# Kernel tuning notes

Measured on AMD Instinct MI355X. Metric: run time of the kernel, lower is better.

## Reference

```python
import jax, jax.numpy as jnp
import numpy as np

N = 100_000   # nodes
E = 1_200_000 # edges
D = 64        # in_dim
H = 64        # hidden_dim
B = 1000      # graphs in batch
C = 10        # num_classes
TOPO = 64     # topo_dim
BN_EPS = 1e-5


def setup_inputs() -> dict:
    key = jax.random.key(0)
    ks = jax.random.split(key, 24)
    x = jax.random.normal(ks[0], (N, D), dtype=jnp.float32)
    edge_index = jax.random.randint(ks[1], (2, E), 0, N, dtype=jnp.int32)
    # sorted graph ids; force last id = B-1 so batch.max()+1 == B (matches torch path)
    batch = jnp.sort(jax.random.randint(ks[2], (N,), 0, B, dtype=jnp.int32)).at[-1].set(B - 1)
    topo = jax.random.normal(ks[3], (B, TOPO), dtype=jnp.float32)
    s = 0.05
    return {
        "x": x, "edge_index": edge_index, "batch": batch, "topo": topo,
        # conv1 MLP: Linear(D,H) -> BN(H) -> ReLU -> Linear(H,H) -> ReLU
        "W1a": jax.random.normal(ks[4], (D, H)) * s, "b1a": jax.random.normal(ks[5], (H,)) * s,
        "g1": 1.0 + jax.random.normal(ks[6], (H,)) * s, "be1": jax.random.normal(ks[7], (H,)) * s,
        "m1": jax.random.normal(ks[8], (H,)) * s, "v1": 0.5 + jax.random.uniform(ks[9], (H,)),
        "W1b": jax.random.normal(ks[10], (H, H)) * s, "b1b": jax.random.normal(ks[11], (H,)) * s,
        # conv2 MLP: Linear(H,H) -> BN(H) -> ReLU
        "W2": jax.random.normal(ks[12], (H, H)) * s, "b2": jax.random.normal(ks[13], (H,)) * s,
        "g2": 1.0 + jax.random.normal(ks[14], (H,)) * s, "be2": jax.random.normal(ks[15], (H,)) * s,
        "m2": jax.random.normal(ks[16], (H,)) * s, "v2": 0.5 + jax.random.uniform(ks[17], (H,)),
        # topo_net: Linear(TOPO,H) -> ReLU
        "Wt": jax.random.normal(ks[18], (TOPO, H)) * s, "bt": jax.random.normal(ks[19], (H,)) * s,
        # classifier: Linear(2H, C)
        "Wc": jax.random.normal(ks[20], (2 * H, C)) * s, "bc": jax.random.normal(ks[21], (C,)) * s,
    }


def _bn_eval(v, g, b, m, var):
    # BatchNorm1d in eval mode: affine with running stats
    return g * (v - m) * jax.lax.rsqrt(var + BN_EPS) + b


def _gin_agg(h, src, dst):
    # GINConv (eps=0): (1+eps)*x_i + sum_{j->i} x_j ; scatter-add over dst
    return h + jax.ops.segment_sum(h[src], dst, num_segments=N)


def reference(x, edge_index, batch, topo,
              W1a, b1a, g1, be1, m1, v1, W1b, b1b,
              W2, b2, g2, be2, m2, v2, Wt, bt, Wc, bc):
    src, dst = edge_index[0], edge_index[1]
    # conv1: MLP(agg(x)) = Lin -> BN -> ReLU -> Lin -> ReLU; outer relu from forward
    h = _gin_agg(x, src, dst)                              # [N, D]
    h = jax.nn.relu(_bn_eval(h @ W1a + b1a, g1, be1, m1, v1))
    h = jax.nn.relu(h @ W1b + b1b)                         # [N, H]
    h = jax.nn.relu(h)                                     # F.relu(conv1(...))
    # dropout(p=0.5) is identity in eval mode
    # conv2: Lin -> BN -> ReLU, then outer relu
    h = _gin_agg(h, src, dst)                              # [N, H]
    h = jax.nn.relu(_bn_eval(h @ W2 + b2, g2, be2, m2, v2))
    h = jax.nn.relu(h)
    # global_add_pool: sum nodes per graph
    x_struct = jax.ops.segment_sum(h, batch, num_segments=B)   # [B, H]
    # topo already [B, TOPO] => all reshape/pad branches are no-ops
    x_topo = jax.nn.relu(topo @ Wt + bt)                   # [B, H]
    combined = jnp.concatenate([x_struct, x_topo], axis=1) # [B, 2H]
    return combined @ Wc + bc                              # [B, C]
```

## Files before the change

kernel.cpp:

```cpp
#include <hip/hip_runtime.h>

#define N_NODES 100000
#define N_EDGES 1200000
#define DIM     64
#define BGRAPHS 1000
#define NCLASS  10
#define BN_EPS  1e-5f

#define NBUCK   256
#define NPB     391
#define MAGIC   10984572u
#define CHUNK   8192
#define NBLK_P  147
#define SCAN_N  (NBUCK * NBLK_P)
#define CAP     8192

typedef __attribute__((ext_vector_type(8))) short   bfx8;
typedef __attribute__((ext_vector_type(4))) float   f32x4;
typedef __attribute__((ext_vector_type(8))) unsigned short u16x8;

__device__ __forceinline__ unsigned short f2bf(float f) {
    unsigned u = __builtin_bit_cast(unsigned, f);
    unsigned r = (u + 0x7FFFu + ((u >> 16) & 1u)) >> 16;
    return (unsigned short)r;
}
__device__ __forceinline__ float bf2f(unsigned short h) {
    unsigned u = ((unsigned)h) << 16;
    return __builtin_bit_cast(float, u);
}

__global__ void convert_kernel(const float* __restrict__ x, unsigned short* __restrict__ xb,
                               float* __restrict__ xs) {
    int i = blockIdx.x * blockDim.x + threadIdx.x;
    const int n8 = N_NODES * DIM / 8;
    if (i < n8) {
        float4 a = ((const float4*)x)[i * 2];
        float4 b = ((const float4*)x)[i * 2 + 1];
        u16x8 o;
        o[0] = f2bf(a.x); o[1] = f2bf(a.y); o[2] = f2bf(a.z); o[3] = f2bf(a.w);
        o[4] = f2bf(b.x); o[5] = f2bf(b.y); o[6] = f2bf(b.z); o[7] = f2bf(b.w);
        ((u16x8*)xb)[i] = o;
    }
    if (i < BGRAPHS * DIM) xs[i] = 0.f;
}

__global__ __launch_bounds__(256) void histA_kernel(const int* __restrict__ ei,
                                                    int* __restrict__ hist) {
    __shared__ int cnt[NBUCK];
    int t = threadIdx.x, blk = blockIdx.x;
    cnt[t] = 0;
    __syncthreads();
    int e0 = blk * CHUNK;
    for (int i = t; i < CHUNK; i += 256) {
        int e = e0 + i;
        if (e >= N_EDGES) break;
        unsigned d = (unsigned)ei[N_EDGES + e];
        int b = __umulhi(d, MAGIC);
        atomicAdd(&cnt[b], 1);
    }
    __syncthreads();
    hist[t * NBLK_P + blk] = cnt[t];
}

__global__ __launch_bounds__(256) void scan1_kernel(const int* __restrict__ in,
                                                    int* __restrict__ outp,
                                                    int* __restrict__ bsum, int n) {
    __shared__ int tmp[256];
    int t = threadIdx.x;
    int base = blockIdx.x * 1024;
    int v[4]; int s = 0;
    #pragma unroll
    for (int j = 0; j < 4; ++j) {
        int idx = base + t * 4 + j;
        v[j] = (idx < n) ? in[idx] : 0;
        s += v[j];
    }
    tmp[t] = s;
    __syncthreads();
    for (int off = 1; off < 256; off <<= 1) {
        int a = (t >= off) ? tmp[t - off] : 0;
        __syncthreads();
        tmp[t] += a;
        __syncthreads();
    }
    int excl = tmp[t] - s;
    if (t == 255) bsum[blockIdx.x] = tmp[255];
    int run = excl;
    #pragma unroll
    for (int j = 0; j < 4; ++j) {
        int idx = base + t * 4 + j;
        if (idx < n) outp[idx] = run;
        run += v[j];
    }
}

__global__ __launch_bounds__(128) void scan2_kernel(int* __restrict__ bsum, int nb) {
    __shared__ int tmp[128];
    int t = threadIdx.x;
    int v = (t < nb) ? bsum[t] : 0;
    tmp[t] = v;
    __syncthreads();
    for (int off = 1; off < 128; off <<= 1) {
        int a = (t >= off) ? tmp[t - off] : 0;
        __syncthreads();
        tmp[t] += a;
        __syncthreads();
    }
    if (t < nb) bsum[t] = tmp[t] - v;
}

__global__ void scan3_kernel(int* __restrict__ arr, const int* __restrict__ bsum, int n) {
    int i = blockIdx.x * blockDim.x + threadIdx.x;
    if (i < n) arr[i] += bsum[i >> 10];
}

__global__ __launch_bounds__(256) void part_kernel(const int* __restrict__ ei,
                                                   const int* __restrict__ base,
                                                   int* __restrict__ srcbuf,
                                                   unsigned short* __restrict__ dstlbuf) {
    __shared__ int cur[NBUCK];
    int t = threadIdx.x, blk = blockIdx.x;
    cur[t] = base[t * NBLK_P + blk];
    __syncthreads();
    int e0 = blk * CHUNK;
    for (int i = t; i < CHUNK; i += 256) {
        int e = e0 + i;
        if (e >= N_EDGES) break;
        unsigned d = (unsigned)ei[N_EDGES + e];
        int s = ei[e];
        int b = __umulhi(d, MAGIC);
        int pos = atomicAdd(&cur[b], 1);
        srcbuf[pos] = s;
        dstlbuf[pos] = (unsigned short)(d - b * NPB);
    }
}

__global__ __launch_bounds__(256) void refine_kernel(const int* __restrict__ srcbuf,
                                                     const unsigned short* __restrict__ dstlbuf,
                                                     const int* __restrict__ base,
                                                     int* __restrict__ csr_src,
                                                     int* __restrict__ rowptr) {
    __shared__ int cnt[NPB + 1];
    __shared__ int cur[NPB + 1];
    __shared__ int tmp[256];
    __shared__ int outb[CAP];
    int t = threadIdx.x, b = blockIdx.x;
    int beg = base[b * NBLK_P];
    int end = (b == NBUCK - 1) ? N_EDGES : base[(b + 1) * NBLK_P];

    for (int i = t; i < NPB + 1; i += 256) cnt[i] = 0;
    __syncthreads();
    for (int i = beg + t; i < end; i += 256)
        atomicAdd(&cnt[dstlbuf[i]], 1);
    __syncthreads();

    int i0 = 2 * t, i1 = 2 * t + 1;
    int v0 = (i0 < NPB) ? cnt[i0] : 0;
    int v1 = (i1 < NPB) ? cnt[i1] : 0;
    int s = v0 + v1;
    tmp[t] = s;
    __syncthreads();
    for (int off = 1; off < 256; off <<= 1) {
        int a = (t >= off) ? tmp[t - off] : 0;
        __syncthreads();
        tmp[t] += a;
        __syncthreads();
    }
    int excl = tmp[t] - s;
    if (i0 < NPB) cur[i0] = excl;
    if (i1 < NPB) cur[i1] = excl + v0;
    {
        int g0 = b * NPB + i0;
        if (i0 < NPB && g0 < N_NODES) rowptr[g0] = beg + excl;
        int g1 = b * NPB + i1;
        if (i1 < NPB && g1 < N_NODES) rowptr[g1] = beg + excl + v0;
    }
    if (b == NBUCK - 1 && t == 0) rowptr[N_NODES] = N_EDGES;
    __syncthreads();

    for (int i = beg + t; i < end; i += 256) {
        int dl = dstlbuf[i];
        int pos = atomicAdd(&cur[dl], 1);
        if (pos < CAP) outb[pos] = srcbuf[i];
    }
    __syncthreads();

    int nb = end - beg; if (nb > CAP) nb = CAP;
    for (int i = t; i < nb; i += 256) csr_src[beg + i] = outb[i];
}

__global__ __launch_bounds__(256) void gather_kernel(const unsigned short* __restrict__ feat,
                                                     const int* __restrict__ rowptr,
                                                     const int* __restrict__ csr_src,
                                                     unsigned short* __restrict__ out) {
    int t = threadIdx.x;
    int node = blockIdx.x * 32 + (t >> 3);
    int q = t & 7;
    if (node >= N_NODES) return;
    const u16x8* f8 = (const u16x8*)feat;
    u16x8 sv = f8[(long long)node * 8 + q];
    float acc[8];
    #pragma unroll
    for (int j = 0; j < 8; ++j) acc[j] = bf2f(sv[j]);
    int beg = rowptr[node], end = rowptr[node + 1];
    int k = beg;
    int sn = (k < end) ? csr_src[k] : 0;
    while (k < end) {
        int sc = sn;
        ++k;
        if (k < end) sn = csr_src[k];
        u16x8 v = f8[(long long)sc * 8 + q];
        #pragma unroll
        for (int j = 0; j < 8; ++j) acc[j] += bf2f(v[j]);
    }
    u16x8 o;
    #pragma unroll
    for (int j = 0; j < 8; ++j) o[j] = f2bf(acc[j]);
    ((u16x8*)out)[(long long)node * 8 + q] = o;
}

__device__ __forceinline__ bfx8 load_wfrag(const float* __restrict__ W, int kt, int q, int col) {
    bfx8 f;
    #pragma unroll
    for (int j = 0; j < 8; ++j)
        f[j] = (short)f2bf(W[(kt * 32 + q * 8 + j) * 64 + col]);
    return f;
}

__global__ __launch_bounds__(256) void mlp1_kernel(
    const unsigned short* __restrict__ h0,
    const float* __restrict__ W1a, const float* __restrict__ b1a,
    const float* __restrict__ g1,  const float* __restrict__ be1,
    const float* __restrict__ m1,  const float* __restrict__ v1,
    const float* __restrict__ W1b, const float* __restrict__ b1b,
    unsigned short* __restrict__ h2) {
    __shared__ unsigned short h1t[4][16 * 72];
    __shared__ unsigned short outt[4][16 * 64];

    int t = threadIdx.x;
    int w = t >> 6, lane = t & 63;
    int m = lane & 15, q = lane >> 4;
    int row0 = blockIdx.x * 64 + w * 16;

    bfx8 wa[4][2], wb[4][2];
    #pragma unroll
    for (int nt = 0; nt < 4; ++nt) {
        #pragma unroll
        for (int kt = 0; kt < 2; ++kt) {
            wa[nt][kt] = load_wfrag(W1a, kt, q, nt * 16 + m);
            wb[nt][kt] = load_wfrag(W1b, kt, q, nt * 16 + m);
        }
    }
    float A1[4], B1[4], B2c[4];
    #pragma unroll
    for (int nt = 0; nt < 4; ++nt) {
        int c = nt * 16 + m;
        float s = g1[c] * rsqrtf(v1[c] + BN_EPS);
        A1[nt] = s;
        B1[nt] = b1a[c] * s + (be1[c] - m1[c] * s);
        B2c[nt] = b1b[c];
    }

    int rowA = row0 + m;
    if (rowA > N_NODES - 1) rowA = N_NODES - 1;
    const bfx8* ap = (const bfx8*)(h0 + (long long)rowA * 64);
    bfx8 a0 = ap[q];
    bfx8 a1 = ap[4 + q];
    f32x4 acc[4];
    #pragma unroll
    for (int nt = 0; nt < 4; ++nt) {
        acc[nt] = (f32x4){0.f, 0.f, 0.f, 0.f};
        acc[nt] = __builtin_amdgcn_mfma_f32_16x16x32_bf16(a0, wa[nt][0], acc[nt], 0, 0, 0);
        acc[nt] = __builtin_amdgcn_mfma_f32_16x16x32_bf16(a1, wa[nt][1], acc[nt], 0, 0, 0);
    }
    #pragma unroll
    for (int nt = 0; nt < 4; ++nt)
        #pragma unroll
        for (int r = 0; r < 4; ++r) {
            float v = fmaxf(acc[nt][r] * A1[nt] + B1[nt], 0.f);
            h1t[w][(q * 4 + r) * 72 + nt * 16 + m] = f2bf(v);
        }
    __syncthreads();

    const bfx8* hp = (const bfx8*)&h1t[w][m * 72];
    bfx8 c0 = hp[q];
    bfx8 c1 = hp[4 + q];
    f32x4 acc2[4];
    #pragma unroll
    for (int nt = 0; nt < 4; ++nt) {
        acc2[nt] = (f32x4){0.f, 0.f, 0.f, 0.f};
        acc2[nt] = __builtin_amdgcn_mfma_f32_16x16x32_bf16(c0, wb[nt][0], acc2[nt], 0, 0, 0);
        acc2[nt] = __builtin_amdgcn_mfma_f32_16x16x32_bf16(c1, wb[nt][1], acc2[nt], 0, 0, 0);
    }
    #pragma unroll
    for (int nt = 0; nt < 4; ++nt)
        #pragma unroll
        for (int r = 0; r < 4; ++r) {
            float v = fmaxf(acc2[nt][r] + B2c[nt], 0.f);
            outt[w][(q * 4 + r) * 64 + nt * 16 + m] = f2bf(v);
        }
    __syncthreads();

    #pragma unroll
    for (int i = lane; i < 128; i += 64) {
        int rr = i >> 3, cc = i & 7;
        int rg = row0 + rr;
        if (rg < N_NODES)
            ((float4*)h2)[(long long)rg * 8 + cc] = *(const float4*)&outt[w][rr * 64 + cc * 8];
    }
}

__global__ __launch_bounds__(256) void mlp2_kernel(
    const unsigned short* __restrict__ h3,
    const float* __restrict__ W2, const float* __restrict__ b2,
    const float* __restrict__ g2, const float* __restrict__ be2,
    const float* __restrict__ m2, const float* __restrict__ v2,
    const int* __restrict__ batch,
    float* __restrict__ xs) {
    __shared__ float pool[64 * 64];
    __shared__ int bts[64];

    int t = threadIdx.x;
    int w = t >> 6, lane = t & 63;
    int m = lane & 15, q = lane >> 4;
    int row0b = blockIdx.x * 64;
    int row0 = row0b + w * 16;

    bfx8 wf[4][2];
    #pragma unroll
    for (int nt = 0; nt < 4; ++nt)
        #pragma unroll
        for (int kt = 0; kt < 2; ++kt)
            wf[nt][kt] = load_wfrag(W2, kt, q, nt * 16 + m);
    float A[4], Bc[4];
    #pragma unroll
    for (int nt = 0; nt < 4; ++nt) {
        int c = nt * 16 + m;
        float s = g2[c] * rsqrtf(v2[c] + BN_EPS);
        A[nt] = s;
        Bc[nt] = b2[c] * s + (be2[c] - m2[c] * s);
    }
    if (t < 64) {
        int rg = row0b + t;
        bts[t] = (rg < N_NODES) ? batch[rg] : -1;
    }

    int rowA = row0 + m;
    if (rowA > N_NODES - 1) rowA = N_NODES - 1;
    const bfx8* ap = (const bfx8*)(h3 + (long long)rowA * 64);
    bfx8 a0 = ap[q];
    bfx8 a1 = ap[4 + q];
    f32x4 acc[4];
    #pragma unroll
    for (int nt = 0; nt < 4; ++nt) {
        acc[nt] = (f32x4){0.f, 0.f, 0.f, 0.f};
        acc[nt] = __builtin_amdgcn_mfma_f32_16x16x32_bf16(a0, wf[nt][0], acc[nt], 0, 0, 0);
        acc[nt] = __builtin_amdgcn_mfma_f32_16x16x32_bf16(a1, wf[nt][1], acc[nt], 0, 0, 0);
    }
    #pragma unroll
    for (int nt = 0; nt < 4; ++nt)
        #pragma unroll
        for (int r = 0; r < 4; ++r) {
            float v = fmaxf(acc[nt][r] * A[nt] + Bc[nt], 0.f);
            pool[(w * 16 + q * 4 + r) * 64 + nt * 16 + m] = v;
        }
    __syncthreads();

    int col = t & 63;
    int r0 = (t >> 6) * 16;
    int cb = bts[r0];
    float cur = 0.f;
    #pragma unroll
    for (int r = 0; r < 16; ++r) {
        int b = bts[r0 + r];
        if (b != cb) {
            if (cb >= 0) unsafeAtomicAdd(&xs[cb * 64 + col], cur);
            cb = b;
            cur = 0.f;
        }
        cur += pool[(r0 + r) * 64 + col];
    }
    if (cb >= 0) unsafeAtomicAdd(&xs[cb * 64 + col], cur);
}

__global__ __launch_bounds__(64) void head_kernel(
    const float* __restrict__ xs, const float* __restrict__ topo,
    const float* __restrict__ Wt, const float* __restrict__ bt,
    const float* __restrict__ Wc, const float* __restrict__ bc,
    float* __restrict__ out) {
    __shared__ float trow[64];
    __shared__ float comb[128];
    int b = blockIdx.x;
    int h = threadIdx.x;
    trow[h] = topo[b * 64 + h];
    __syncthreads();
    float acc = bt[h];
    #pragma unroll
    for (int k = 0; k < 64; ++k) acc += trow[k] * Wt[k * 64 + h];
    comb[h] = xs[b * 64 + h];
    comb[64 + h] = fmaxf(acc, 0.f);
    __syncthreads();
    if (h < NCLASS) {
        float o = bc[h];
        #pragma unroll
        for (int k = 0; k < 128; ++k) o += comb[k] * Wc[k * NCLASS + h];
        out[b * NCLASS + h] = o;
    }
}

extern "C" void kernel_launch(void* const* d_in, const int* in_sizes, int n_in,
                              void* d_out, int out_size, void* d_ws, size_t ws_size,
                              hipStream_t stream) {
    const float* x     = (const float*)d_in[0];
    const int*   ei    = (const int*)d_in[1];
    const int*   batch = (const int*)d_in[2];
    const float* topo  = (const float*)d_in[3];
    const float* W1a   = (const float*)d_in[4];
    const float* b1a   = (const float*)d_in[5];
    const float* g1    = (const float*)d_in[6];
    const float* be1   = (const float*)d_in[7];
    const float* m1    = (const float*)d_in[8];
    const float* v1    = (const float*)d_in[9];
    const float* W1b   = (const float*)d_in[10];
    const float* b1b   = (const float*)d_in[11];
    const float* W2    = (const float*)d_in[12];
    const float* b2    = (const float*)d_in[13];
    const float* g2    = (const float*)d_in[14];
    const float* be2   = (const float*)d_in[15];
    const float* m2    = (const float*)d_in[16];
    const float* v2    = (const float*)d_in[17];
    const float* Wt    = (const float*)d_in[18];
    const float* bt    = (const float*)d_in[19];
    const float* Wc    = (const float*)d_in[20];
    const float* bc    = (const float*)d_in[21];
    float* out = (float*)d_out;

    char* p = (char*)d_ws;
    unsigned short* xbf  = (unsigned short*)p; p += (size_t)N_NODES * DIM * 2;
    unsigned short* bufA = (unsigned short*)p; p += (size_t)N_NODES * DIM * 2;
    unsigned short* bufB = (unsigned short*)p; p += (size_t)N_NODES * DIM * 2;
    float* xs      = (float*)p; p += (size_t)BGRAPHS * DIM * 4;
    int*   rowptr  = (int*)p;   p += (size_t)(N_NODES + 16) * 4;
    int*   histc   = (int*)p;   p += (size_t)SCAN_N * 4;
    int*   base    = (int*)p;   p += (size_t)SCAN_N * 4;
    int*   bsum    = (int*)p;   p += 256 * 4;
    int*   srcbuf  = (int*)p;   p += (size_t)N_EDGES * 4;
    unsigned short* dstlbuf = (unsigned short*)p; p += (size_t)N_EDGES * 2;
    int*   csr_src = (int*)p;

    const int NB_C  = (N_NODES * DIM / 8 + 255) / 256;
    const int NB_S1 = (SCAN_N + 1023) / 1024;
    const int NB_S3 = (SCAN_N + 255) / 256;

    convert_kernel<<<NB_C, 256, 0, stream>>>(x, xbf, xs);
    histA_kernel<<<NBLK_P, 256, 0, stream>>>(ei, histc);
    scan1_kernel<<<NB_S1, 256, 0, stream>>>(histc, base, bsum, SCAN_N);
    scan2_kernel<<<1, 128, 0, stream>>>(bsum, NB_S1);
    scan3_kernel<<<NB_S3, 256, 0, stream>>>(base, bsum, SCAN_N);
    part_kernel<<<NBLK_P, 256, 0, stream>>>(ei, base, srcbuf, dstlbuf);
    refine_kernel<<<NBUCK, 256, 0, stream>>>(srcbuf, dstlbuf, base, csr_src, rowptr);

    gather_kernel<<<(N_NODES + 31) / 32, 256, 0, stream>>>(xbf, rowptr, csr_src, bufA);
    mlp1_kernel<<<(N_NODES + 63) / 64, 256, 0, stream>>>(
        bufA, W1a, b1a, g1, be1, m1, v1, W1b, b1b, bufB);
    gather_kernel<<<(N_NODES + 31) / 32, 256, 0, stream>>>(bufB, rowptr, csr_src, bufA);
    mlp2_kernel<<<(N_NODES + 63) / 64, 256, 0, stream>>>(
        bufA, W2, b2, g2, be2, m2, v2, batch, xs);
    head_kernel<<<BGRAPHS, 64, 0, stream>>>(xs, topo, Wt, bt, Wc, bc, out);
}
```

Baseline: 246.8 us.

## Fuse neighbor gather into MLP kernels and collapse CSR scan pipeline

Removes the standalone gather kernels and performs the CSR neighbor aggregation directly inside mlp1/mlp2, so the aggregated bf16 rows no longer round-trip through global memory. Each MFMA row lane now gathers 16 features across two 8-wide chunks, unrolled by two edges. Separately, the bf16 convert and edge histogram are merged into one launch, and the three-kernel scan is replaced by a single bucket-level scan plus atomic cursors in part_kernel. This cuts launches and intermediate traffic. In exchange, edge order within buckets becomes nondeterministic and gather parallelism per node drops (4 lanes instead of 8), which may expose more latency.

```diff
diff --git a/kernel.cpp b/kernel.cpp
--- a/kernel.cpp
+++ b/kernel.cpp
@@ -12,8 +12,8 @@
 #define MAGIC   10984572u
 #define CHUNK   8192
 #define NBLK_P  147
-#define SCAN_N  (NBUCK * NBLK_P)
 #define CAP     8192
+#define NB_C    3125
 
 typedef __attribute__((ext_vector_type(8))) short   bfx8;
 typedef __attribute__((ext_vector_type(4))) float   f32x4;
@@ -29,24 +29,67 @@
     return __builtin_bit_cast(float, u);
 }
 
-__global__ void convert_kernel(const float* __restrict__ x, unsigned short* __restrict__ xb,
-                               float* __restrict__ xs) {
-    int i = blockIdx.x * blockDim.x + threadIdx.x;
-    const int n8 = N_NODES * DIM / 8;
-    if (i < n8) {
-        float4 a = ((const float4*)x)[i * 2];
-        float4 b = ((const float4*)x)[i * 2 + 1];
-        u16x8 o;
-        o[0] = f2bf(a.x); o[1] = f2bf(a.y); o[2] = f2bf(a.z); o[3] = f2bf(a.w);
-        o[4] = f2bf(b.x); o[5] = f2bf(b.y); o[6] = f2bf(b.z); o[7] = f2bf(b.w);
-        ((u16x8*)xb)[i] = o;
-    }
-    if (i < BGRAPHS * DIM) xs[i] = 0.f;
-}
-
-__global__ __launch_bounds__(256) void histA_kernel(const int* __restrict__ ei,
-                                                    int* __restrict__ hist) {
+__global__ __launch_bounds__(256) void convhist_kernel(
+    const float* __restrict__ x, unsigned short* __restrict__ xb,
+    float* __restrict__ xs, const int* __restrict__ ei,
+    int* __restrict__ gpart) {
     __shared__ int cnt[NBUCK];
+    int t = threadIdx.x;
+    if (blockIdx.x < NBLK_P) {
+        int blk = blockIdx.x;
+        cnt[t] = 0;
+        __syncthreads();
+        int e0 = blk * CHUNK;
+        for (int i = t; i < CHUNK; i += 256) {
+            int e = e0 + i;
+            if (e >= N_EDGES) break;
+            unsigned d = (unsigned)ei[N_EDGES + e];
+            atomicAdd(&cnt[__umulhi(d, MAGIC)], 1);
+        }
+        __syncthreads();
+        gpart[blk * NBUCK + t] = cnt[t];
+    } else {
+        int i = (blockIdx.x - NBLK_P) * 256 + t;
+        const int n8 = N_NODES * DIM / 8;
+        if (i < n8) {
+            float4 a = ((const float4*)x)[i * 2];
+            float4 b = ((const float4*)x)[i * 2 + 1];
+            u16x8 o;
+            o[0] = f2bf(a.x); o[1] = f2bf(a.y); o[2] = f2bf(a.z); o[3] = f2bf(a.w);
+            o[4] = f2bf(b.x); o[5] = f2bf(b.y); o[6] = f2bf(b.z); o[7] = f2bf(b.w);
+            ((u16x8*)xb)[i] = o;
+        }
+        if (i < BGRAPHS * DIM) xs[i] = 0.f;
+    }
+}
+
+__global__ __launch_bounds__(256) void scanB_kernel(const int* __restrict__ gpart,
+                                                    int* __restrict__ base,
+                                                    int* __restrict__ cursor) {
+    __shared__ int tmp[256];
+    int t = threadIdx.x;
+    int s = 0;
+    for (int blk = 0; blk < NBLK_P; ++blk) s += gpart[blk * NBUCK + t];
+    tmp[t] = s;
+    __syncthreads();
+    for (int off = 1; off < 256; off <<= 1) {
+        int a = (t >= off) ? tmp[t - off] : 0;
+        __syncthreads();
+        tmp[t] += a;
+        __syncthreads();
+    }
+    int excl = tmp[t] - s;
+    base[t] = excl;
+    cursor[t] = excl;
+    if (t == 255) base[256] = N_EDGES;
+}
+
+__global__ __launch_bounds__(256) void part_kernel(const int* __restrict__ ei,
+                                                   int* __restrict__ cursor,
+                                                   int* __restrict__ srcbuf,
+                                                   unsigned short* __restrict__ dstlbuf) {
+    __shared__ int cnt[NBUCK];
+    __shared__ int cur[NBUCK];
     int t = threadIdx.x, blk = blockIdx.x;
     cnt[t] = 0;
     __syncthreads();
@@ -55,74 +98,11 @@
         int e = e0 + i;
         if (e >= N_EDGES) break;
         unsigned d = (unsigned)ei[N_EDGES + e];
-        int b = __umulhi(d, MAGIC);
-        atomicAdd(&cnt[b], 1);
-    }
-    __syncthreads();
-    hist[t * NBLK_P + blk] = cnt[t];
-}
-
-__global__ __launch_bounds__(256) void scan1_kernel(const int* __restrict__ in,
-                                                    int* __restrict__ outp,
-                                                    int* __restrict__ bsum, int n) {
-    __shared__ int tmp[256];
-    int t = threadIdx.x;
-    int base = blockIdx.x * 1024;
-    int v[4]; int s = 0;
-    #pragma unroll
-    for (int j = 0; j < 4; ++j) {
-        int idx = base + t * 4 + j;
-        v[j] = (idx < n) ? in[idx] : 0;
-        s += v[j];
-    }
-    tmp[t] = s;
-    __syncthreads();
-    for (int off = 1; off < 256; off <<= 1) {
-        int a = (t >= off) ? tmp[t - off] : 0;
-        __syncthreads();
-        tmp[t] += a;
-        __syncthreads();
-    }
-    int excl = tmp[t] - s;
-    if (t == 255) bsum[blockIdx.x] = tmp[255];
-    int run = excl;
-    #pragma unroll
-    for (int j = 0; j < 4; ++j) {
-        int idx = base + t * 4 + j;
-        if (idx < n) outp[idx] = run;
-        run += v[j];
-    }
-}
-
-__global__ __launch_bounds__(128) void scan2_kernel(int* __restrict__ bsum, int nb) {
-    __shared__ int tmp[128];
-    int t = threadIdx.x;
-    int v = (t < nb) ? bsum[t] : 0;
-    tmp[t] = v;
-    __syncthreads();
-    for (int off = 1; off < 128; off <<= 1) {
-        int a = (t >= off) ? tmp[t - off] : 0;
-        __syncthreads();
-        tmp[t] += a;
-        __syncthreads();
-    }
-    if (t < nb) bsum[t] = tmp[t] - v;
-}
-
-__global__ void scan3_kernel(int* __restrict__ arr, const int* __restrict__ bsum, int n) {
-    int i = blockIdx.x * blockDim.x + threadIdx.x;
-    if (i < n) arr[i] += bsum[i >> 10];
-}
-
-__global__ __launch_bounds__(256) void part_kernel(const int* __restrict__ ei,
-                                                   const int* __restrict__ base,
-                                                   int* __restrict__ srcbuf,
-                                                   unsigned short* __restrict__ dstlbuf) {
-    __shared__ int cur[NBUCK];
-    int t = threadIdx.x, blk = blockIdx.x;
-    cur[t] = base[t * NBLK_P + blk];
-    __syncthreads();
-    int e0 = blk * CHUNK;
+        atomicAdd(&cnt[__umulhi(d, MAGIC)], 1);
+    }
+    __syncthreads();
+    cur[t] = atomicAdd(&cursor[t], cnt[t]);
+    __syncthreads();
     for (int i = t; i < CHUNK; i += 256) {
         int e = e0 + i;
         if (e >= N_EDGES) break;
@@ -145,8 +125,8 @@
     __shared__ int tmp[256];
     __shared__ int outb[CAP];
     int t = threadIdx.x, b = blockIdx.x;
-    int beg = base[b * NBLK_P];
-    int end = (b == NBUCK - 1) ? N_EDGES : base[(b + 1) * NBLK_P];
+    int beg = base[b];
+    int end = base[b + 1];
 
     for (int i = t; i < NPB + 1; i += 256) cnt[i] = 0;
     __syncthreads();
@@ -189,34 +169,39 @@
     for (int i = t; i < nb; i += 256) csr_src[beg + i] = outb[i];
 }
 
-__global__ __launch_bounds__(256) void gather_kernel(const unsigned short* __restrict__ feat,
-                                                     const int* __restrict__ rowptr,
-                                                     const int* __restrict__ csr_src,
-                                                     unsigned short* __restrict__ out) {
-    int t = threadIdx.x;
-    int node = blockIdx.x * 32 + (t >> 3);
-    int q = t & 7;
-    if (node >= N_NODES) return;
+__device__ __forceinline__ void gather_row(const unsigned short* __restrict__ feat,
+                                           const int* __restrict__ rowptr,
+                                           const int* __restrict__ csr_src,
+                                           int rowA, int q,
+                                           float* accl, float* acch) {
     const u16x8* f8 = (const u16x8*)feat;
-    u16x8 sv = f8[(long long)node * 8 + q];
-    float acc[8];
-    #pragma unroll
-    for (int j = 0; j < 8; ++j) acc[j] = bf2f(sv[j]);
-    int beg = rowptr[node], end = rowptr[node + 1];
-    int k = beg;
-    int sn = (k < end) ? csr_src[k] : 0;
-    while (k < end) {
-        int sc = sn;
-        ++k;
-        if (k < end) sn = csr_src[k];
-        u16x8 v = f8[(long long)sc * 8 + q];
-        #pragma unroll
-        for (int j = 0; j < 8; ++j) acc[j] += bf2f(v[j]);
-    }
-    u16x8 o;
-    #pragma unroll
-    for (int j = 0; j < 8; ++j) o[j] = f2bf(acc[j]);
-    ((u16x8*)out)[(long long)node * 8 + q] = o;
+    u16x8 s0 = f8[(long long)rowA * 8 + q];
+    u16x8 s1 = f8[(long long)rowA * 8 + 4 + q];
+    #pragma unroll
+    for (int j = 0; j < 8; ++j) { accl[j] = bf2f(s0[j]); acch[j] = bf2f(s1[j]); }
+    int k = rowptr[rowA], end = rowptr[rowA + 1];
+    for (; k + 2 <= end; k += 2) {
+        int sa = csr_src[k], sb = csr_src[k + 1];
+        u16x8 va0 = f8[(long long)sa * 8 + q];
+        u16x8 va1 = f8[(long long)sa * 8 + 4 + q];
+        u16x8 vb0 = f8[(long long)sb * 8 + q];
+        u16x8 vb1 = f8[(long long)sb * 8 + 4 + q];
+        #pragma unroll
+        for (int j = 0; j < 8; ++j) {
+            accl[j] += bf2f(va0[j]) + bf2f(vb0[j]);
+            acch[j] += bf2f(va1[j]) + bf2f(vb1[j]);
+        }
+    }
+    if (k < end) {
+        int sa = csr_src[k];
+        u16x8 va0 = f8[(long long)sa * 8 + q];
+        u16x8 va1 = f8[(long long)sa * 8 + 4 + q];
+        #pragma unroll
+        for (int j = 0; j < 8; ++j) {
+            accl[j] += bf2f(va0[j]);
+            acch[j] += bf2f(va1[j]);
+        }
+    }
 }
 
 __device__ __forceinline__ bfx8 load_wfrag(const float* __restrict__ W, int kt, int q, int col) {
@@ -228,7 +213,8 @@
 }
 
 __global__ __launch_bounds__(256) void mlp1_kernel(
-    const unsigned short* __restrict__ h0,
+    const unsigned short* __restrict__ xbf,
+    const int* __restrict__ rowptr, const int* __restrict__ csr_src,
     const float* __restrict__ W1a, const float* __restrict__ b1a,
     const float* __restrict__ g1,  const float* __restrict__ be1,
     const float* __restrict__ m1,  const float* __restrict__ v1,
@@ -263,9 +249,15 @@
 
     int rowA = row0 + m;
     if (rowA > N_NODES - 1) rowA = N_NODES - 1;
-    const bfx8* ap = (const bfx8*)(h0 + (long long)rowA * 64);
-    bfx8 a0 = ap[q];
-    bfx8 a1 = ap[4 + q];
+    float accl[8], acch[8];
+    gather_row(xbf, rowptr, csr_src, rowA, q, accl, acch);
+    bfx8 a0, a1;
+    #pragma unroll
+    for (int j = 0; j < 8; ++j) {
+        a0[j] = (short)f2bf(accl[j]);
+        a1[j] = (short)f2bf(acch[j]);
+    }
+
     f32x4 acc[4];
     #pragma unroll
     for (int nt = 0; nt < 4; ++nt) {
@@ -311,7 +303,8 @@
 }
 
 __global__ __launch_bounds__(256) void mlp2_kernel(
-    const unsigned short* __restrict__ h3,
+    const unsigned short* __restrict__ h2,
+    const int* __restrict__ rowptr, const int* __restrict__ csr_src,
     const float* __restrict__ W2, const float* __restrict__ b2,
     const float* __restrict__ g2, const float* __restrict__ be2,
     const float* __restrict__ m2, const float* __restrict__ v2,
@@ -347,9 +340,15 @@
 
     int rowA = row0 + m;
     if (rowA > N_NODES - 1) rowA = N_NODES - 1;
-    const bfx8* ap = (const bfx8*)(h3 + (long long)rowA * 64);
-    bfx8 a0 = ap[q];
-    bfx8 a1 = ap[4 + q];
+    float accl[8], acch[8];
+    gather_row(h2, rowptr, csr_src, rowA, q, accl, acch);
+    bfx8 a0, a1;
+    #pragma unroll
+    for (int j = 0; j < 8; ++j) {
+        a0[j] = (short)f2bf(accl[j]);
+        a1[j] = (short)f2bf(acch[j]);
+    }
+
     f32x4 acc[4];
     #pragma unroll
     for (int nt = 0; nt < 4; ++nt) {
@@ -437,34 +436,23 @@
 
     char* p = (char*)d_ws;
     unsigned short* xbf  = (unsigned short*)p; p += (size_t)N_NODES * DIM * 2;
-    unsigned short* bufA = (unsigned short*)p; p += (size_t)N_NODES * DIM * 2;
     unsigned short* bufB = (unsigned short*)p; p += (size_t)N_NODES * DIM * 2;
     float* xs      = (float*)p; p += (size_t)BGRAPHS * DIM * 4;
     int*   rowptr  = (int*)p;   p += (size_t)(N_NODES + 16) * 4;
-    int*   histc   = (int*)p;   p += (size_t)SCAN_N * 4;
-    int*   base    = (int*)p;   p += (size_t)SCAN_N * 4;
-    int*   bsum    = (int*)p;   p += 256 * 4;
+    int*   gpart   = (int*)p;   p += (size_t)NBLK_P * NBUCK * 4;
+    int*   base    = (int*)p;   p += 1040;
+    int*   cursor  = (int*)p;   p += 1024;
     int*   srcbuf  = (int*)p;   p += (size_t)N_EDGES * 4;
     unsigned short* dstlbuf = (unsigned short*)p; p += (size_t)N_EDGES * 2;
     int*   csr_src = (int*)p;
 
-    const int NB_C  = (N_NODES * DIM / 8 + 255) / 256;
-    const int NB_S1 = (SCAN_N + 1023) / 1024;
-    const int NB_S3 = (SCAN_N + 255) / 256;
-
-    convert_kernel<<<NB_C, 256, 0, stream>>>(x, xbf, xs);
-    histA_kernel<<<NBLK_P, 256, 0, stream>>>(ei, histc);
-    scan1_kernel<<<NB_S1, 256, 0, stream>>>(histc, base, bsum, SCAN_N);
-    scan2_kernel<<<1, 128, 0, stream>>>(bsum, NB_S1);
-    scan3_kernel<<<NB_S3, 256, 0, stream>>>(base, bsum, SCAN_N);
-    part_kernel<<<NBLK_P, 256, 0, stream>>>(ei, base, srcbuf, dstlbuf);
+    convhist_kernel<<<NBLK_P + NB_C, 256, 0, stream>>>(x, xbf, xs, ei, gpart);
+    scanB_kernel<<<1, 256, 0, stream>>>(gpart, base, cursor);
+    part_kernel<<<NBLK_P, 256, 0, stream>>>(ei, cursor, srcbuf, dstlbuf);
     refine_kernel<<<NBUCK, 256, 0, stream>>>(srcbuf, dstlbuf, base, csr_src, rowptr);
-
-    gather_kernel<<<(N_NODES + 31) / 32, 256, 0, stream>>>(xbf, rowptr, csr_src, bufA);
     mlp1_kernel<<<(N_NODES + 63) / 64, 256, 0, stream>>>(
-        bufA, W1a, b1a, g1, be1, m1, v1, W1b, b1b, bufB);
-    gather_kernel<<<(N_NODES + 31) / 32, 256, 0, stream>>>(bufB, rowptr, csr_src, bufA);
+        xbf, rowptr, csr_src, W1a, b1a, g1, be1, m1, v1, W1b, b1b, bufB);
     mlp2_kernel<<<(N_NODES + 63) / 64, 256, 0, stream>>>(
-        bufA, W2, b2, g2, be2, m2, v2, batch, xs);
+        bufB, rowptr, csr_src, W2, b2, g2, be2, m2, v2, batch, xs);
     head_kernel<<<BGRAPHS, 64, 0, stream>>>(xs, topo, Wt, bt, Wc, bc, out);
 }
```

Result: slower. 274.1 us (+11.1%).
